# Kernel optimization log

Measured on AMD Instinct MI355X. Metric: run time of the kernel, lower is better.

Reference implementation:

```python
import jax, jax.numpy as jnp
import numpy as np

B = 2048   # batch
D = 1280   # backbone feature dim (hardcoded in module)
E = 8      # num_classes == number of expert heads
ALPHA = 0.1
EPS = 1e-5


def _bn(x, g, b, m, v):
    # BatchNorm1d in eval mode: running stats
    return (x - m) * jax.lax.rsqrt(v + EPS) * g + b


def _ln(x, g, b):
    mu = jnp.mean(x, axis=-1, keepdims=True)
    var = jnp.mean((x - mu) ** 2, axis=-1, keepdims=True)
    return (x - mu) * jax.lax.rsqrt(var + EPS) * g + b


@jax.custom_vjp
def _grad_reverse(x):
    return x

def _gr_fwd(x):
    return x, None

def _gr_bwd(_, g):
    return (-ALPHA * g,)

_grad_reverse.defvjp(_gr_fwd, _gr_bwd)


def setup_inputs() -> dict:
    key = jax.random.key(0)
    ks = iter(jax.random.split(key, 80))
    def w(*s):
        return jax.random.normal(next(ks), s, dtype=jnp.float32) * 0.02
    def u(*s):
        return jax.random.uniform(next(ks), s, dtype=jnp.float32) + 0.5
    inp = {"source": jax.random.normal(next(ks), (B, D), dtype=jnp.float32)}
    # bottleneck: Linear(1280,512)+BN+ReLU, Linear(512,256)+BN+ReLU
    inp.update(bw1=w(D, 512), bb1=jnp.zeros(512), bg1=jnp.ones(512), bbe1=jnp.zeros(512), bm1=w(512), bv1=u(512))
    inp.update(bw2=w(512, 256), bb2=jnp.zeros(256), bg2=jnp.ones(256), bbe2=jnp.zeros(256), bm2=w(256), bv2=u(256))
    # source_fc: Linear(256, E) + LogSoftmax
    inp.update(cw=w(256, E), cb=jnp.zeros(E))
    # domain classifier: 1280->1024->1024->512->2 with BN
    inp.update(dw1=w(D, 1024), db1=jnp.zeros(1024), dg1=jnp.ones(1024), dbe1=jnp.zeros(1024), dm1=w(1024), dv1=u(1024))
    inp.update(dw2=w(1024, 1024), db2=jnp.zeros(1024), dg2=jnp.ones(1024), dbe2=jnp.zeros(1024), dm2=w(1024), dv2=u(1024))
    inp.update(dw3=w(1024, 512), db3=jnp.zeros(512), dg3=jnp.ones(512), dbe3=jnp.zeros(512), dm3=w(512), dv3=u(512))
    inp.update(dw4=w(512, 2), db4=jnp.zeros(2))
    # E stacked expert MLPs: 1280->1024->1024->512->2 with LayerNorm
    inp.update(ew1=w(E, D, 1024), eb1=jnp.zeros((E, 1024)), eg1=jnp.ones((E, 1024)), ebe1=jnp.zeros((E, 1024)))
    inp.update(ew2=w(E, 1024, 1024), eb2=jnp.zeros((E, 1024)), eg2=jnp.ones((E, 1024)), ebe2=jnp.zeros((E, 1024)))
    inp.update(ew3=w(E, 1024, 512), eb3=jnp.zeros((E, 512)), eg3=jnp.ones((E, 512)), ebe3=jnp.zeros((E, 512)))
    inp.update(ew4=w(E, 512, 2), eb4=jnp.zeros((E, 2)))
    return inp


def reference(source, bw1, bb1, bg1, bbe1, bm1, bv1, bw2, bb2, bg2, bbe2, bm2, bv2, cw, cb,
              dw1, db1, dg1, dbe1, dm1, dv1, dw2, db2, dg2, dbe2, dm2, dv2,
              dw3, db3, dg3, dbe3, dm3, dv3, dw4, db4,
              ew1, eb1, eg1, ebe1, ew2, eb2, eg2, ebe2, ew3, eb3, eg3, ebe3, ew4, eb4):
    share = source  # sharedNet modeled as identity on extracted features
    # bottleneck + classifier head
    h = jax.nn.relu(_bn(share @ bw1 + bb1, bg1, bbe1, bm1, bv1))
    h = jax.nn.relu(_bn(h @ bw2 + bb2, bg2, bbe2, bm2, bv2))
    src = jax.nn.log_softmax(h @ cw + cb, axis=-1)            # [B, E]
    label = jnp.argmax(src, axis=-1)                          # routing labels (detached by argmax)
    # gradient-reversed features
    rev = _grad_reverse(share)
    # global domain classifier (dropout = identity in eval)
    d = jax.nn.relu(_bn(rev @ dw1 + db1, dg1, dbe1, dm1, dv1))
    d = jax.nn.relu(_bn(d @ dw2 + db2, dg2, dbe2, dm2, dv2))
    d = jax.nn.relu(_bn(d @ dw3 + db3, dg3, dbe3, dm3, dv3))
    dclf = jax.nn.log_softmax(d @ dw4 + db4, axis=-1)         # [B, 2]
    # per-class domain experts: dense all-expert compute + per-sample gather
    x = jax.nn.relu(_ln(jnp.einsum('bd,edh->beh', rev, ew1) + eb1[None], eg1[None], ebe1[None]))
    x = jax.nn.relu(_ln(jnp.einsum('beh,ehk->bek', x, ew2) + eb2[None], eg2[None], ebe2[None]))
    x = jax.nn.relu(_ln(jnp.einsum('beh,ehk->bek', x, ew3) + eb3[None], eg3[None], ebe3[None]))
    eo = jax.nn.log_softmax(jnp.einsum('beh,ehk->bek', x, ew4) + eb4[None], axis=-1)  # [B, E, 2]
    sout = jnp.take_along_axis(eo, label[:, None, None], axis=1)[:, 0, :]             # [B, 2]
    return (src, dclf, sout, share)
```

## Files before the change

### kernel.cpp

```cpp
#include <hip/hip_runtime.h>

typedef unsigned short u16;
typedef short s8v __attribute__((ext_vector_type(8)));
typedef float f4v __attribute__((ext_vector_type(4)));

#define AS1 __attribute__((address_space(1)))
#define AS3 __attribute__((address_space(3)))

__device__ __forceinline__ float bf2f(u16 u) {
    union { unsigned int i; float f; } x; x.i = ((unsigned int)u) << 16; return x.f;
}
__device__ __forceinline__ u16 f2bf(float f) {
    union { float f; unsigned int i; } x; x.f = f;
    unsigned int r = x.i + 0x7fffu + ((x.i >> 16) & 1u);
    return (u16)(r >> 16);
}

__device__ __forceinline__ void glds16(const u16* g, u16* l) {
    __builtin_amdgcn_global_load_lds((AS1 void*)(g), (AS3 void*)(l), 16, 0, 0);
}

__device__ __forceinline__ int swz(int row, int kq) {
    return row * 64 + ((((kq >> 3) ^ row) & 7) << 3);
}

__global__ __launch_bounds__(256) void convT2_k(const float* __restrict__ Wa,
        const float* __restrict__ Wb, int zSplit,
        u16* __restrict__ WT, int N, int K)
{
    const int z = blockIdx.z;
    const float* W = (z < zSplit) ? Wa + (size_t)z * K * N
                                  : Wb + (size_t)(z - zSplit) * K * N;
    WT += (size_t)z * K * N;
    const int n0 = blockIdx.x * 64, k0 = blockIdx.y * 64;
    __shared__ float t[64][65];
    const int r = threadIdx.x >> 2;
    const int c = (threadIdx.x & 3) << 4;
    const float* wp = W + (size_t)(k0 + r) * N + n0 + c;
    #pragma unroll
    for (int q = 0; q < 16; q += 4) {
        float4 f = *(const float4*)(wp + q);
        t[c + q + 0][r] = f.x; t[c + q + 1][r] = f.y;
        t[c + q + 2][r] = f.z; t[c + q + 3][r] = f.w;
    }
    __syncthreads();
    u16* op = WT + (size_t)(n0 + r) * K + k0 + c;
    #pragma unroll
    for (int q = 0; q < 16; q += 8) {
        s8v v;
        #pragma unroll
        for (int j = 0; j < 8; ++j) v[j] = (short)f2bf(t[r][c + q + j]);
        *(s8v*)(op + q) = v;
    }
}

__global__ __launch_bounds__(256) void convsrc_k(const float* __restrict__ in,
        u16* __restrict__ outb, float* __restrict__ outf, int n8)
{
    const int i = blockIdx.x * 256 + threadIdx.x;
    if (i >= n8) return;
    const float4 f0 = ((const float4*)in)[i * 2];
    const float4 f1 = ((const float4*)in)[i * 2 + 1];
    s8v v;
    v[0]=(short)f2bf(f0.x); v[1]=(short)f2bf(f0.y);
    v[2]=(short)f2bf(f0.z); v[3]=(short)f2bf(f0.w);
    v[4]=(short)f2bf(f1.x); v[5]=(short)f2bf(f1.y);
    v[6]=(short)f2bf(f1.z); v[7]=(short)f2bf(f1.w);
    ((s8v*)outb)[i] = v;
    ((float4*)outf)[i * 2]     = f0;
    ((float4*)outf)[i * 2 + 1] = f1;
}

template<int HASDOM>
__global__ __launch_bounds__(512) void gemm_bt128_k(
    const u16* __restrict__ A0, size_t aStrideZ,
    const u16* __restrict__ WT0,
    const float* __restrict__ ebias,
    const float* __restrict__ dbias, const float* __restrict__ dgam,
    const float* __restrict__ dbet,  const float* __restrict__ dmean,
    const float* __restrict__ dvar,  int zdom,
    u16* __restrict__ out0, int M, int N, int K)
{
    const int z = blockIdx.z;
    const u16* A  = A0  + (size_t)z * aStrideZ;
    const u16* WT = WT0 + (size_t)z * N * K;
    u16* out = out0 + (size_t)z * M * N;

    const int n0 = blockIdx.x * 128, m0 = blockIdx.y * 128;
    const int t = threadIdx.x;
    const int w = t >> 6, lane = t & 63;
    const int lq = lane >> 4, lr = lane & 15;
    const int wm = (w >> 1) * 32;
    const int wn = (w & 1) * 64;

    __shared__ __align__(16) u16 As[2 * 128 * 64];
    __shared__ __align__(16) u16 Bs[2 * 128 * 64];

    f4v acc[2][4] = {};

    const int srow = t >> 3;
    const u16* ga = A  + (size_t)(m0 + srow) * K + (((t & 7) ^ (srow & 7)) << 3);
    const u16* gb = WT + (size_t)(n0 + srow) * K + (((t & 7) ^ (srow & 7)) << 3);
    const int wq = w * 512;
    const int rowK = 64 * K;

#define STAGE(buf, kk) do { \
    glds16(ga + (kk),        As + (buf) * 8192 + wq); \
    glds16(ga + (kk) + rowK, As + (buf) * 8192 + 4096 + wq); \
    glds16(gb + (kk),        Bs + (buf) * 8192 + wq); \
    glds16(gb + (kk) + rowK, Bs + (buf) * 8192 + 4096 + wq); \
  } while (0)

    const int NT = K >> 6;
    STAGE(0, 0);
    STAGE(1, 64);

    for (int tk = 0; tk < NT; ++tk) {
        if (tk < NT - 1) asm volatile("s_waitcnt vmcnt(4)" ::: "memory");
        else             asm volatile("s_waitcnt vmcnt(0)" ::: "memory");
        __builtin_amdgcn_s_barrier();
        __builtin_amdgcn_sched_barrier(0);

        const u16* Ah = As + (tk & 1) * 8192;
        const u16* Bh = Bs + (tk & 1) * 8192;
        __builtin_amdgcn_s_setprio(1);
        #pragma unroll
        for (int ks = 0; ks < 64; ks += 32) {
            const int kq = ks + (lq << 3);
            s8v a[2], b[4];
            #pragma unroll
            for (int i = 0; i < 2; ++i) a[i] = *(const s8v*)&Ah[swz(wm + i*16 + lr, kq)];
            #pragma unroll
            for (int j = 0; j < 4; ++j) b[j] = *(const s8v*)&Bh[swz(wn + j*16 + lr, kq)];
            #pragma unroll
            for (int i = 0; i < 2; ++i)
                #pragma unroll
                for (int j = 0; j < 4; ++j)
                    acc[i][j] = __builtin_amdgcn_mfma_f32_16x16x32_bf16(a[i], b[j], acc[i][j], 0, 0, 0);
        }
        __builtin_amdgcn_s_setprio(0);
        __builtin_amdgcn_sched_barrier(0);
        __builtin_amdgcn_s_barrier();

        if (tk + 2 < NT)
            STAGE(tk & 1, (tk + 2) << 6);
    }
#undef STAGE

    float scale[4], shift[4];
    const bool dom = HASDOM && (z == zdom);
    #pragma unroll
    for (int j = 0; j < 4; ++j) {
        const int c = n0 + wn + j * 16 + lr;
        if (dom) {
            const float s = dgam[c] / sqrtf(dvar[c] + 1e-5f);
            scale[j] = s;
            shift[j] = (dbias[c] - dmean[c]) * s + dbet[c];
        } else {
            scale[j] = 1.f;
            shift[j] = ebias[(size_t)z * N + c];
        }
    }
    const int r0 = lq << 2;
    #pragma unroll
    for (int i = 0; i < 2; ++i) {
        #pragma unroll
        for (int r = 0; r < 4; ++r) {
            const int grow = m0 + wm + i * 16 + r0 + r;
            u16* orow = out + (size_t)grow * N + n0 + wn + lr;
            #pragma unroll
            for (int j = 0; j < 4; ++j) {
                float y = fmaf(acc[i][j][r], scale[j], shift[j]);
                if (dom) y = fmaxf(y, 0.f);
                orow[j * 16] = f2bf(y);
            }
        }
    }
}

__global__ __launch_bounds__(256) void gemm_f32sk_k(
    const float* __restrict__ A, const float* __restrict__ W,
    float* __restrict__ out, int M, int N, int K, int Ks)
{
    const int n0 = blockIdx.x * 128, m0 = blockIdx.y * 64;
    const int kb = blockIdx.z * Ks;
    out += (size_t)blockIdx.z * M * N;
    const int t = threadIdx.x;
    const int tx = t & 15, ty = t >> 4;
    __shared__ float As[64 * 33];
    __shared__ float Bs[32 * 132];
    float acc[4][8] = {};
    const int ar = t >> 2, akc = (t & 3) * 8;
    const int bk = t >> 3, bnc = (t & 7) * 16;
    for (int kk = kb; kk < kb + Ks; kk += 32) {
        const float* ap = A + (size_t)(m0 + ar) * K + kk + akc;
        const float4 fa0 = *(const float4*)(ap);
        const float4 fa1 = *(const float4*)(ap + 4);
        float* asp = &As[ar * 33 + akc];
        asp[0] = fa0.x; asp[1] = fa0.y; asp[2] = fa0.z; asp[3] = fa0.w;
        asp[4] = fa1.x; asp[5] = fa1.y; asp[6] = fa1.z; asp[7] = fa1.w;
        const float* wp = W + (size_t)(kk + bk) * N + n0 + bnc;
        #pragma unroll
        for (int q = 0; q < 4; ++q)
            *(float4*)&Bs[bk * 132 + bnc + q * 4] = *(const float4*)(wp + q * 4);
        __syncthreads();
        #pragma unroll 8
        for (int kq = 0; kq < 32; ++kq) {
            float a[4];
            #pragma unroll
            for (int i = 0; i < 4; ++i) a[i] = As[(ty + 16 * i) * 33 + kq];
            const float4 b0 = *(const float4*)&Bs[kq * 132 + tx * 4];
            const float4 b1 = *(const float4*)&Bs[kq * 132 + tx * 4 + 64];
            #pragma unroll
            for (int i = 0; i < 4; ++i) {
                acc[i][0] = fmaf(a[i], b0.x, acc[i][0]);
                acc[i][1] = fmaf(a[i], b0.y, acc[i][1]);
                acc[i][2] = fmaf(a[i], b0.z, acc[i][2]);
                acc[i][3] = fmaf(a[i], b0.w, acc[i][3]);
                acc[i][4] = fmaf(a[i], b1.x, acc[i][4]);
                acc[i][5] = fmaf(a[i], b1.y, acc[i][5]);
                acc[i][6] = fmaf(a[i], b1.z, acc[i][6]);
                acc[i][7] = fmaf(a[i], b1.w, acc[i][7]);
            }
        }
        __syncthreads();
    }
    #pragma unroll
    for (int i = 0; i < 4; ++i) {
        float* orow = out + (size_t)(m0 + ty + 16 * i) * N + n0 + tx * 4;
        float4 o0; o0.x = acc[i][0]; o0.y = acc[i][1]; o0.z = acc[i][2]; o0.w = acc[i][3];
        float4 o1; o1.x = acc[i][4]; o1.y = acc[i][5]; o1.z = acc[i][6]; o1.w = acc[i][7];
        *(float4*)orow = o0;
        *(float4*)(orow + 64) = o1;
    }
}

__global__ __launch_bounds__(256) void h2gemm_k(
    const float* __restrict__ hp,
    const float* __restrict__ bg1, const float* __restrict__ bbe1,
    const float* __restrict__ bb1, const float* __restrict__ bm1,
    const float* __restrict__ bv1,
    const float* __restrict__ bw2,
    float* __restrict__ out, int B)
{
    const int n0 = blockIdx.x * 64, m0 = blockIdx.y * 64;
    const int kb = blockIdx.z * 128;
    out += (size_t)blockIdx.z * B * 256;
    const size_t sl = (size_t)B * 512;
    const int tid = threadIdx.x;
    const int tx = tid & 15, ty = tid >> 4;
    __shared__ float As[64][65];
    __shared__ float Bs[64][64];
    __shared__ __align__(16) float scl[128], shl[128];
    if (tid < 128) {
        const int k = kb + tid;
        const float sc = bg1[k] / sqrtf(bv1[k] + 1e-5f);
        scl[tid] = sc;
        shl[tid] = (bb1[k] - bm1[k]) * sc + bbe1[k];
    }
    __syncthreads();
    float acc[4][4] = {};
    const int sr = tid >> 2;
    const int sc = (tid & 3) << 4;
    for (int kk = kb; kk < kb + 128; kk += 64) {
        const int kl = kk - kb;
        const float* ap = hp + (size_t)(m0 + sr) * 512 + kk + sc;
        #pragma unroll
        for (int q = 0; q < 4; ++q) {
            float vx = 0.f, vy = 0.f, vz = 0.f, vw = 0.f;
            #pragma unroll
            for (int s = 0; s < 8; ++s) {
                const float4 f = *(const float4*)(ap + (size_t)s * sl + q * 4);
                vx += f.x; vy += f.y; vz += f.z; vw += f.w;
            }
            const float4 g = *(const float4*)&scl[kl + sc + q * 4];
            const float4 h = *(const float4*)&shl[kl + sc + q * 4];
            As[sr][sc + q*4 + 0] = fmaxf(fmaf(vx, g.x, h.x), 0.f);
            As[sr][sc + q*4 + 1] = fmaxf(fmaf(vy, g.y, h.y), 0.f);
            As[sr][sc + q*4 + 2] = fmaxf(fmaf(vz, g.z, h.z), 0.f);
            As[sr][sc + q*4 + 3] = fmaxf(fmaf(vw, g.w, h.w), 0.f);
        }
        const float* wp = bw2 + (size_t)(kk + sr) * 256 + n0 + sc;
        #pragma unroll
        for (int q = 0; q < 4; ++q)
            *(float4*)&Bs[sr][sc + q*4] = *(const float4*)(wp + q * 4);
        __syncthreads();
        #pragma unroll 4
        for (int kq = 0; kq < 64; ++kq) {
            float a[4], bv[4];
            #pragma unroll
            for (int i = 0; i < 4; ++i) a[i] = As[ty*4 + i][kq];
            #pragma unroll
            for (int j = 0; j < 4; ++j) bv[j] = Bs[kq][tx*4 + j];
            #pragma unroll
            for (int i = 0; i < 4; ++i)
                #pragma unroll
                for (int j = 0; j < 4; ++j)
                    acc[i][j] = fmaf(a[i], bv[j], acc[i][j]);
        }
        __syncthreads();
    }
    #pragma unroll
    for (int j = 0; j < 4; ++j) {
        const int c = n0 + tx*4 + j;
        #pragma unroll
        for (int i = 0; i < 4; ++i)
            out[(size_t)(m0 + ty*4 + i) * 256 + c] = acc[i][j];
    }
}

__global__ __launch_bounds__(256) void cls_k(
    const float* __restrict__ h2p,
    const float* __restrict__ bg2, const float* __restrict__ bbe2,
    const float* __restrict__ bb2, const float* __restrict__ bm2,
    const float* __restrict__ bv2,
    const float* __restrict__ cw,  const float* __restrict__ cb,
    float* __restrict__ out_src, int* __restrict__ label, int B)
{
    const int b = blockIdx.x * 4 + (threadIdx.x >> 6);
    const int lane = threadIdx.x & 63;
    const size_t sl = (size_t)B * 256;
    const float* hb = h2p + (size_t)b * 256 + lane * 4;
    const float4 v0 = *(const float4*)(hb);
    const float4 v1 = *(const float4*)(hb + sl);
    const float4 v2 = *(const float4*)(hb + 2 * sl);
    const float4 v3 = *(const float4*)(hb + 3 * sl);
    const float4 gv = ((const float4*)bg2)[lane];
    const float4 vv = ((const float4*)bv2)[lane];
    const float4 bbv = ((const float4*)bb2)[lane];
    const float4 bmv = ((const float4*)bm2)[lane];
    const float4 bev = ((const float4*)bbe2)[lane];
    float h[4];
    {
        const float s0 = gv.x / sqrtf(vv.x + 1e-5f);
        const float s1 = gv.y / sqrtf(vv.y + 1e-5f);
        const float s2 = gv.z / sqrtf(vv.z + 1e-5f);
        const float s3 = gv.w / sqrtf(vv.w + 1e-5f);
        h[0] = fmaxf(fmaf(v0.x + v1.x + v2.x + v3.x, s0, (bbv.x - bmv.x) * s0 + bev.x), 0.f);
        h[1] = fmaxf(fmaf(v0.y + v1.y + v2.y + v3.y, s1, (bbv.y - bmv.y) * s1 + bev.y), 0.f);
        h[2] = fmaxf(fmaf(v0.z + v1.z + v2.z + v3.z, s2, (bbv.z - bmv.z) * s2 + bev.z), 0.f);
        h[3] = fmaxf(fmaf(v0.w + v1.w + v2.w + v3.w, s3, (bbv.w - bmv.w) * s3 + bev.w), 0.f);
    }
    float p[8] = {};
    #pragma unroll
    for (int j = 0; j < 4; ++j) {
        const float4 c0 = ((const float4*)cw)[(lane * 4 + j) * 2];
        const float4 c1 = ((const float4*)cw)[(lane * 4 + j) * 2 + 1];
        p[0] = fmaf(h[j], c0.x, p[0]); p[1] = fmaf(h[j], c0.y, p[1]);
        p[2] = fmaf(h[j], c0.z, p[2]); p[3] = fmaf(h[j], c0.w, p[3]);
        p[4] = fmaf(h[j], c1.x, p[4]); p[5] = fmaf(h[j], c1.y, p[5]);
        p[6] = fmaf(h[j], c1.z, p[6]); p[7] = fmaf(h[j], c1.w, p[7]);
    }
    #pragma unroll
    for (int off = 32; off; off >>= 1)
        #pragma unroll
        for (int c = 0; c < 8; ++c) p[c] += __shfl_xor(p[c], off, 64);
    if (lane == 0) {
        float lg[8];
        #pragma unroll
        for (int c = 0; c < 8; ++c) lg[c] = p[c] + cb[c];
        float mx = lg[0]; int am = 0;
        #pragma unroll
        for (int c = 1; c < 8; ++c) if (lg[c] > mx) { mx = lg[c]; am = c; }
        float ssum = 0.f;
        #pragma unroll
        for (int c = 0; c < 8; ++c) ssum += expf(lg[c] - mx);
        const float lse = mx + logf(ssum);
        #pragma unroll
        for (int c = 0; c < 8; ++c) out_src[b * 8 + c] = lg[c] - lse;
        label[b] = am;
    }
}

template<int N>
__global__ __launch_bounds__(256) void ln_relu_k(u16* __restrict__ Y,
        const float* __restrict__ g, const float* __restrict__ bb)
{
    const int z = blockIdx.y;
    u16* y = Y + ((size_t)z * gridDim.x + blockIdx.x) * N;
    const float* gz = g  + (size_t)z * N;
    const float* bz = bb + (size_t)z * N;
    const int t = threadIdx.x;
    constexpr int C = N >> 8;
    float vals[C];
    ushort4 u = ((const ushort4*)y)[t];
    vals[0] = bf2f(u.x); vals[1] = bf2f(u.y);
    vals[2] = bf2f(u.z); vals[3] = bf2f(u.w);
    float s = 0.f, sq = 0.f;
    #pragma unroll
    for (int i = 0; i < C; ++i) { s += vals[i]; sq += vals[i] * vals[i]; }
    #pragma unroll
    for (int off = 32; off; off >>= 1) {
        s  += __shfl_xor(s,  off, 64);
        sq += __shfl_xor(sq, off, 64);
    }
    __shared__ float rs[4], rq[4];
    if ((t & 63) == 0) { rs[t >> 6] = s; rq[t >> 6] = sq; }
    __syncthreads();
    s  = rs[0] + rs[1] + rs[2] + rs[3];
    sq = rq[0] + rq[1] + rq[2] + rq[3];
    const float inv = 1.f / (float)N;
    const float mu  = s * inv;
    const float var = sq * inv - mu * mu;
    const float rstd = rsqrtf(var + 1e-5f);
    float4 gv = ((const float4*)gz)[t];
    float4 bv = ((const float4*)bz)[t];
    ushort4 o;
    o.x = f2bf(fmaxf((vals[0] - mu) * rstd * gv.x + bv.x, 0.f));
    o.y = f2bf(fmaxf((vals[1] - mu) * rstd * gv.y + bv.y, 0.f));
    o.z = f2bf(fmaxf((vals[2] - mu) * rstd * gv.z + bv.z, 0.f));
    o.w = f2bf(fmaxf((vals[3] - mu) * rstd * gv.w + bv.w, 0.f));
    ((ushort4*)y)[t] = o;
}

__global__ __launch_bounds__(64) void headsel_k(
    const u16* __restrict__ X,
    const int* __restrict__ label,
    const float* __restrict__ eg3, const float* __restrict__ ebe3,
    const float* __restrict__ ew4, const float* __restrict__ eb4,
    int zBase, float* __restrict__ out_sout, int B)
{
    const int b = blockIdx.x;
    const int e = label[b];
    if (e < zBase || e >= zBase + 4) return;
    const int lane = threadIdx.x;
    const u16* x = X + ((size_t)(e - zBase) * B + b) * 512 + lane * 8;
    uint4 raw = *(const uint4*)x;
    const u16* pu = (const u16*)&raw;
    float v[8];
    #pragma unroll
    for (int i = 0; i < 8; ++i) v[i] = bf2f(pu[i]);
    float s = 0.f, sq = 0.f;
    #pragma unroll
    for (int i = 0; i < 8; ++i) { s += v[i]; sq += v[i] * v[i]; }
    #pragma unroll
    for (int off = 32; off; off >>= 1) {
        s  += __shfl_xor(s,  off, 64);
        sq += __shfl_xor(sq, off, 64);
    }
    const float mu = s * (1.f / 512.f);
    const float var = sq * (1.f / 512.f) - mu * mu;
    const float rstd = rsqrtf(var + 1e-5f);
    const float* g  = eg3  + (size_t)e * 512 + lane * 8;
    const float* be = ebe3 + (size_t)e * 512 + lane * 8;
    const float4 g0 = *(const float4*)g,  g1 = *(const float4*)(g + 4);
    const float4 b0 = *(const float4*)be, b1 = *(const float4*)(be + 4);
    float h[8];
    h[0] = fmaxf((v[0]-mu)*rstd*g0.x + b0.x, 0.f);
    h[1] = fmaxf((v[1]-mu)*rstd*g0.y + b0.y, 0.f);
    h[2] = fmaxf((v[2]-mu)*rstd*g0.z + b0.z, 0.f);
    h[3] = fmaxf((v[3]-mu)*rstd*g0.w + b0.w, 0.f);
    h[4] = fmaxf((v[4]-mu)*rstd*g1.x + b1.x, 0.f);
    h[5] = fmaxf((v[5]-mu)*rstd*g1.y + b1.y, 0.f);
    h[6] = fmaxf((v[6]-mu)*rstd*g1.z + b1.z, 0.f);
    h[7] = fmaxf((v[7]-mu)*rstd*g1.w + b1.w, 0.f);
    const float* W = ew4 + (size_t)e * 1024 + lane * 16;
    float p0 = 0.f, p1 = 0.f;
    #pragma unroll
    for (int q = 0; q < 4; ++q) {
        const float4 wv = *(const float4*)(W + q * 4);
        p0 = fmaf(h[q*2],   wv.x, p0); p1 = fmaf(h[q*2],   wv.y, p1);
        p0 = fmaf(h[q*2+1], wv.z, p0); p1 = fmaf(h[q*2+1], wv.w, p1);
    }
    #pragma unroll
    for (int off = 32; off; off >>= 1) {
        p0 += __shfl_xor(p0, off, 64);
        p1 += __shfl_xor(p1, off, 64);
    }
    if (lane == 0) {
        const float l0 = p0 + eb4[e * 2];
        const float l1 = p1 + eb4[e * 2 + 1];
        const float mx = fmaxf(l0, l1);
        const float lse = mx + logf(expf(l0 - mx) + expf(l1 - mx));
        out_sout[b * 2]     = l0 - lse;
        out_sout[b * 2 + 1] = l1 - lse;
    }
}

__global__ __launch_bounds__(64) void head2_k(const u16* __restrict__ X,
        const float* __restrict__ W, const float* __restrict__ bias,
        float* __restrict__ out)
{
    const int b = blockIdx.x;
    const int lane = threadIdx.x;
    const u16* x = X + (size_t)b * 512 + lane * 8;
    uint4 raw = *(const uint4*)x;
    const u16* pu = (const u16*)&raw;
    const float* Wz = W + lane * 16;
    float p0 = 0.f, p1 = 0.f;
    #pragma unroll
    for (int q = 0; q < 4; ++q) {
        const float4 wv = *(const float4*)(Wz + q * 4);
        p0 = fmaf(bf2f(pu[q*2]),   wv.x, p0); p1 = fmaf(bf2f(pu[q*2]),   wv.y, p1);
        p0 = fmaf(bf2f(pu[q*2+1]), wv.z, p0); p1 = fmaf(bf2f(pu[q*2+1]), wv.w, p1);
    }
    #pragma unroll
    for (int off = 32; off; off >>= 1) {
        p0 += __shfl_xor(p0, off, 64);
        p1 += __shfl_xor(p1, off, 64);
    }
    if (lane == 0) {
        const float l0 = p0 + bias[0];
        const float l1 = p1 + bias[1];
        const float mx = fmaxf(l0, l1);
        const float lse = mx + logf(expf(l0 - mx) + expf(l1 - mx));
        out[b * 2]     = l0 - lse;
        out[b * 2 + 1] = l1 - lse;
    }
}


extern "C" void kernel_launch(void* const* d_in, const int* in_sizes, int n_in,
                              void* d_out, int out_size, void* d_ws, size_t ws_size,
                              hipStream_t stream)
{
    const int B = 2048, D = 1280, E = 8;

    const float* src = (const float*)d_in[0];
    const float *bw1 = (const float*)d_in[1],  *bb1 = (const float*)d_in[2],
                *bg1 = (const float*)d_in[3],  *bbe1 = (const float*)d_in[4],
                *bm1 = (const float*)d_in[5],  *bv1 = (const float*)d_in[6];
    const float *bw2 = (const float*)d_in[7],  *bb2 = (const float*)d_in[8],
                *bg2 = (const float*)d_in[9],  *bbe2 = (const float*)d_in[10],
                *bm2 = (const float*)d_in[11], *bv2 = (const float*)d_in[12];
    const float *cw  = (const float*)d_in[13], *cb  = (const float*)d_in[14];
    const float *dw1 = (const float*)d_in[15], *db1 = (const float*)d_in[16],
                *dg1 = (const float*)d_in[17], *dbe1 = (const float*)d_in[18],
                *dm1 = (const float*)d_in[19], *dv1 = (const float*)d_in[20];
    const float *dw2 = (const float*)d_in[21], *db2 = (const float*)d_in[22],
                *dg2 = (const float*)d_in[23], *dbe2 = (const float*)d_in[24],
                *dm2 = (const float*)d_in[25], *dv2 = (const float*)d_in[26];
    const float *dw3 = (const float*)d_in[27], *db3 = (const float*)d_in[28],
                *dg3 = (const float*)d_in[29], *dbe3 = (const float*)d_in[30],
                *dm3 = (const float*)d_in[31], *dv3 = (const float*)d_in[32];
    const float *dw4 = (const float*)d_in[33], *db4 = (const float*)d_in[34];
    const float *ew1 = (const float*)d_in[35], *eb1 = (const float*)d_in[36],
                *eg1 = (const float*)d_in[37], *ebe1 = (const float*)d_in[38];
    const float *ew2 = (const float*)d_in[39], *eb2 = (const float*)d_in[40],
                *eg2 = (const float*)d_in[41], *ebe2 = (const float*)d_in[42];
    const float *ew3 = (const float*)d_in[43], *eb3 = (const float*)d_in[44],
                *eg3 = (const float*)d_in[45], *ebe3 = (const float*)d_in[46];
    const float *ew4 = (const float*)d_in[47], *eb4 = (const float*)d_in[48];

    float* out_src   = (float*)d_out;
    float* out_dclf  = out_src + B * E;
    float* out_sout  = out_dclf + B * 2;
    float* out_share = out_sout + B * 2;

    char* ws = (char*)d_ws;
    u16*   wslot = (u16*)ws;
    u16*   srcb  = (u16*)(ws + 13107200);
    u16*   acta  = (u16*)(ws + 18350080);
    u16*   actb  = (u16*)(ws + 39321600);
    int*   label = (int*)(ws + 60293120);
    float* hp    = (float*)(ws + 18350080);
    float* h2p   = (float*)(ws);

    const size_t s1024 = (size_t)B * 1024, s512 = (size_t)B * 512;

    convsrc_k<<<dim3(B * D / 8 / 256), 256, 0, stream>>>(src, srcb, out_share, B * D / 8);

    gemm_f32sk_k<<<dim3(512 / 128, B / 64, 8), 256, 0, stream>>>(
        src, bw1, hp, B, 512, D, 160);
    h2gemm_k<<<dim3(256 / 64, B / 64, 4), 256, 0, stream>>>(
        hp, bg1, bbe1, bb1, bm1, bv1, bw2, h2p, B);
    cls_k<<<dim3(B / 4), 256, 0, stream>>>(
        h2p, bg2, bbe2, bb2, bm2, bv2, cw, cb, out_src, label, B);

    convT2_k<<<dim3(16, 20, 5), 256, 0, stream>>>(ew1, dw1, 4, wslot, 1024, 1280);
    gemm_bt128_k<1><<<dim3(8, 16, 5), 512, 0, stream>>>(
        srcb, 0, wslot, eb1, db1, dg1, dbe1, dm1, dv1, 4, acta, B, 1024, 1280);
    ln_relu_k<1024><<<dim3(B, 4), 256, 0, stream>>>(acta, eg1, ebe1);

    convT2_k<<<dim3(16, 16, 5), 256, 0, stream>>>(ew2, dw2, 4, wslot, 1024, 1024);
    gemm_bt128_k<1><<<dim3(8, 16, 5), 512, 0, stream>>>(
        acta, s1024, wslot, eb2, db2, dg2, dbe2, dm2, dv2, 4, actb, B, 1024, 1024);
    ln_relu_k<1024><<<dim3(B, 4), 256, 0, stream>>>(actb, eg2, ebe2);

    convT2_k<<<dim3(8, 16, 5), 256, 0, stream>>>(ew3, dw3, 4, wslot, 512, 1024);
    gemm_bt128_k<1><<<dim3(4, 16, 5), 512, 0, stream>>>(
        actb, s1024, wslot, eb3, db3, dg3, dbe3, dm3, dv3, 4, acta, B, 512, 1024);

    headsel_k<<<dim3(B), 64, 0, stream>>>(
        acta, label, eg3, ebe3, ew4, eb4, 0, out_sout, B);
    head2_k<<<dim3(B), 64, 0, stream>>>(
        acta + (size_t)4 * s512, dw4, db4, out_dclf);

    convT2_k<<<dim3(16, 20, 4), 256, 0, stream>>>(
        ew1 + (size_t)4*1280*1024, ew1 + (size_t)4*1280*1024, 4, wslot, 1024, 1280);
    gemm_bt128_k<0><<<dim3(8, 16, 4), 512, 0, stream>>>(
        srcb, 0, wslot, eb1 + (size_t)4*1024,
        nullptr, nullptr, nullptr, nullptr, nullptr, -1, acta, B, 1024, 1280);
    ln_relu_k<1024><<<dim3(B, 4), 256, 0, stream>>>(acta, eg1 + (size_t)4*1024, ebe1 + (size_t)4*1024);

    convT2_k<<<dim3(16, 16, 4), 256, 0, stream>>>(
        ew2 + (size_t)4*1024*1024, ew2 + (size_t)4*1024*1024, 4, wslot, 1024, 1024);
    gemm_bt128_k<0><<<dim3(8, 16, 4), 512, 0, stream>>>(
        acta, s1024, wslot, eb2 + (size_t)4*1024,
        nullptr, nullptr, nullptr, nullptr, nullptr, -1, actb, B, 1024, 1024);
    ln_relu_k<1024><<<dim3(B, 4), 256, 0, stream>>>(actb, eg2 + (size_t)4*1024, ebe2 + (size_t)4*1024);

    convT2_k<<<dim3(8, 16, 4), 256, 0, stream>>>(
        ew3 + (size_t)4*1024*512, ew3 + (size_t)4*1024*512, 4, wslot, 512, 1024);
    gemm_bt128_k<0><<<dim3(4, 16, 4), 512, 0, stream>>>(
        actb, s1024, wslot, eb3 + (size_t)4*512,
        nullptr, nullptr, nullptr, nullptr, nullptr, -1, acta, B, 512, 1024);

    headsel_k<<<dim3(B), 64, 0, stream>>>(
        acta, label, eg3, ebe3, ew4, eb4, 4, out_sout, B);
}
```

Before: 555.3 us.

## Fuse fp32 weight transpose/bf16 conversion into GEMM B-tile loading

Removes the separate convT2_k pre-pass that transposed and converted fp32 weights to bf16 in workspace. The GEMM now reads fp32 weights directly from global memory into registers, converts them to bf16 and writes them into swizzled LDS, with the A tile still loaded asynchronously via global_load_lds. This saves six extra launches and the write and re-read of the bf16 weight copies. In exchange, the pipeline is shallower (one tile ahead instead of two), the strided scalar fp32 loads are each re-read by all 16 M-blocks, and conversion work sits on the GEMM's critical path.

```diff
diff --git a/kernel.cpp b/kernel.cpp
--- a/kernel.cpp
+++ b/kernel.cpp
@@ -22,36 +22,6 @@
 
 __device__ __forceinline__ int swz(int row, int kq) {
     return row * 64 + ((((kq >> 3) ^ row) & 7) << 3);
-}
-
-__global__ __launch_bounds__(256) void convT2_k(const float* __restrict__ Wa,
-        const float* __restrict__ Wb, int zSplit,
-        u16* __restrict__ WT, int N, int K)
-{
-    const int z = blockIdx.z;
-    const float* W = (z < zSplit) ? Wa + (size_t)z * K * N
-                                  : Wb + (size_t)(z - zSplit) * K * N;
-    WT += (size_t)z * K * N;
-    const int n0 = blockIdx.x * 64, k0 = blockIdx.y * 64;
-    __shared__ float t[64][65];
-    const int r = threadIdx.x >> 2;
-    const int c = (threadIdx.x & 3) << 4;
-    const float* wp = W + (size_t)(k0 + r) * N + n0 + c;
-    #pragma unroll
-    for (int q = 0; q < 16; q += 4) {
-        float4 f = *(const float4*)(wp + q);
-        t[c + q + 0][r] = f.x; t[c + q + 1][r] = f.y;
-        t[c + q + 2][r] = f.z; t[c + q + 3][r] = f.w;
-    }
-    __syncthreads();
-    u16* op = WT + (size_t)(n0 + r) * K + k0 + c;
-    #pragma unroll
-    for (int q = 0; q < 16; q += 8) {
-        s8v v;
-        #pragma unroll
-        for (int j = 0; j < 8; ++j) v[j] = (short)f2bf(t[r][c + q + j]);
-        *(s8v*)(op + q) = v;
-    }
 }
 
 __global__ __launch_bounds__(256) void convsrc_k(const float* __restrict__ in,
@@ -72,9 +42,9 @@
 }
 
 template<int HASDOM>
-__global__ __launch_bounds__(512) void gemm_bt128_k(
+__global__ __launch_bounds__(512) void gemm_btf_k(
     const u16* __restrict__ A0, size_t aStrideZ,
-    const u16* __restrict__ WT0,
+    const float* __restrict__ Wa, const float* __restrict__ Wb, int zSplit,
     const float* __restrict__ ebias,
     const float* __restrict__ dbias, const float* __restrict__ dgam,
     const float* __restrict__ dbet,  const float* __restrict__ dmean,
@@ -82,8 +52,9 @@
     u16* __restrict__ out0, int M, int N, int K)
 {
     const int z = blockIdx.z;
-    const u16* A  = A0  + (size_t)z * aStrideZ;
-    const u16* WT = WT0 + (size_t)z * N * K;
+    const u16* A = A0 + (size_t)z * aStrideZ;
+    const float* W = (z < zSplit) ? Wa + (size_t)z * K * N
+                                  : Wb + (size_t)(z - zSplit) * K * N;
     u16* out = out0 + (size_t)z * M * N;
 
     const int n0 = blockIdx.x * 128, m0 = blockIdx.y * 128;
@@ -93,36 +64,62 @@
     const int wm = (w >> 1) * 32;
     const int wn = (w & 1) * 64;
 
-    __shared__ __align__(16) u16 As[2 * 128 * 64];
-    __shared__ __align__(16) u16 Bs[2 * 128 * 64];
+    __shared__ __align__(16) u16 As[2 * 8192];
+    __shared__ __align__(16) u16 Bs[2 * 8192];
 
     f4v acc[2][4] = {};
 
     const int srow = t >> 3;
-    const u16* ga = A  + (size_t)(m0 + srow) * K + (((t & 7) ^ (srow & 7)) << 3);
-    const u16* gb = WT + (size_t)(n0 + srow) * K + (((t & 7) ^ (srow & 7)) << 3);
+    const u16* ga = A + (size_t)(m0 + srow) * K + (((t & 7) ^ (srow & 7)) << 3);
     const int wq = w * 512;
     const int rowK = 64 * K;
 
-#define STAGE(buf, kk) do { \
+#define AGLDS(buf, kk) do { \
     glds16(ga + (kk),        As + (buf) * 8192 + wq); \
-    glds16(ga + (kk) + rowK, As + (buf) * 8192 + 4096 + wq); \
-    glds16(gb + (kk),        Bs + (buf) * 8192 + wq); \
-    glds16(gb + (kk) + rowK, Bs + (buf) * 8192 + 4096 + wq); \
-  } while (0)
+    glds16(ga + (kk) + rowK, As + (buf) * 8192 + 4096 + wq); } while (0)
+
+    const int nl = t & 127;
+    const int kb = (t >> 7) << 4;
+    const float* wp0 = W + (size_t)kb * N + n0 + nl;
+    const int bofs0 = nl * 64 + (((( kb >> 3)      ^ nl) & 7) << 3);
+    const int bofs1 = nl * 64 + (((((kb >> 3) + 1) ^ nl) & 7) << 3);
 
     const int NT = K >> 6;
-    STAGE(0, 0);
-    STAGE(1, 64);
+    float bv[16];
+
+    {
+        #pragma unroll
+        for (int i = 0; i < 16; ++i) bv[i] = wp0[(size_t)i * N];
+        AGLDS(0, 0);
+        s8v pk0, pk1;
+        #pragma unroll
+        for (int i = 0; i < 8; ++i) { pk0[i] = (short)f2bf(bv[i]); pk1[i] = (short)f2bf(bv[8 + i]); }
+        *(s8v*)&Bs[bofs0] = pk0;
+        *(s8v*)&Bs[bofs1] = pk1;
+    }
 
     for (int tk = 0; tk < NT; ++tk) {
-        if (tk < NT - 1) asm volatile("s_waitcnt vmcnt(4)" ::: "memory");
-        else             asm volatile("s_waitcnt vmcnt(0)" ::: "memory");
+        const int cur = tk & 1;
+        if (tk + 1 < NT) {
+            const float* wp = wp0 + (size_t)(tk + 1) * 64 * N;
+            #pragma unroll
+            for (int i = 0; i < 16; ++i) bv[i] = wp[(size_t)i * N];
+            AGLDS(cur ^ 1, (tk + 1) << 6);
+            s8v pk0, pk1;
+            #pragma unroll
+            for (int i = 0; i < 8; ++i) { pk0[i] = (short)f2bf(bv[i]); pk1[i] = (short)f2bf(bv[8 + i]); }
+            u16* bb = Bs + (cur ^ 1) * 8192;
+            *(s8v*)&bb[bofs0] = pk0;
+            *(s8v*)&bb[bofs1] = pk1;
+        } else {
+            asm volatile("s_waitcnt vmcnt(0)" ::: "memory");
+        }
+        asm volatile("s_waitcnt lgkmcnt(0)" ::: "memory");
         __builtin_amdgcn_s_barrier();
         __builtin_amdgcn_sched_barrier(0);
 
-        const u16* Ah = As + (tk & 1) * 8192;
-        const u16* Bh = Bs + (tk & 1) * 8192;
+        const u16* Ah = As + cur * 8192;
+        const u16* Bh = Bs + cur * 8192;
         __builtin_amdgcn_s_setprio(1);
         #pragma unroll
         for (int ks = 0; ks < 64; ks += 32) {
@@ -141,11 +138,8 @@
         __builtin_amdgcn_s_setprio(0);
         __builtin_amdgcn_sched_barrier(0);
         __builtin_amdgcn_s_barrier();
-
-        if (tk + 2 < NT)
-            STAGE(tk & 1, (tk + 2) << 6);
-    }
-#undef STAGE
+    }
+#undef AGLDS
 
     float scale[4], shift[4];
     const bool dom = HASDOM && (z == zdom);
@@ -548,7 +542,6 @@
     float* out_share = out_sout + B * 2;
 
     char* ws = (char*)d_ws;
-    u16*   wslot = (u16*)ws;
     u16*   srcb  = (u16*)(ws + 13107200);
     u16*   acta  = (u16*)(ws + 18350080);
     u16*   actb  = (u16*)(ws + 39321600);
@@ -567,44 +560,38 @@
     cls_k<<<dim3(B / 4), 256, 0, stream>>>(
         h2p, bg2, bbe2, bb2, bm2, bv2, cw, cb, out_src, label, B);
 
-    convT2_k<<<dim3(16, 20, 5), 256, 0, stream>>>(ew1, dw1, 4, wslot, 1024, 1280);
-    gemm_bt128_k<1><<<dim3(8, 16, 5), 512, 0, stream>>>(
-        srcb, 0, wslot, eb1, db1, dg1, dbe1, dm1, dv1, 4, acta, B, 1024, 1280);
+    gemm_btf_k<1><<<dim3(8, 16, 5), 512, 0, stream>>>(
+        srcb, 0, ew1, dw1, 4, eb1, db1, dg1, dbe1, dm1, dv1, 4, acta, B, 1024, 1280);
     ln_relu_k<1024><<<dim3(B, 4), 256, 0, stream>>>(acta, eg1, ebe1);
 
-    convT2_k<<<dim3(16, 16, 5), 256, 0, stream>>>(ew2, dw2, 4, wslot, 1024, 1024);
-    gemm_bt128_k<1><<<dim3(8, 16, 5), 512, 0, stream>>>(
-        acta, s1024, wslot, eb2, db2, dg2, dbe2, dm2, dv2, 4, actb, B, 1024, 1024);
+    gemm_btf_k<1><<<dim3(8, 16, 5), 512, 0, stream>>>(
+        acta, s1024, ew2, dw2, 4, eb2, db2, dg2, dbe2, dm2, dv2, 4, actb, B, 1024, 1024);
     ln_relu_k<1024><<<dim3(B, 4), 256, 0, stream>>>(actb, eg2, ebe2);
 
-    convT2_k<<<dim3(8, 16, 5), 256, 0, stream>>>(ew3, dw3, 4, wslot, 512, 1024);
-    gemm_bt128_k<1><<<dim3(4, 16, 5), 512, 0, stream>>>(
-        actb, s1024, wslot, eb3, db3, dg3, dbe3, dm3, dv3, 4, acta, B, 512, 1024);
+    gemm_btf_k<1><<<dim3(4, 16, 5), 512, 0, stream>>>(
+        actb, s1024, ew3, dw3, 4, eb3, db3, dg3, dbe3, dm3, dv3, 4, acta, B, 512, 1024);
 
     headsel_k<<<dim3(B), 64, 0, stream>>>(
         acta, label, eg3, ebe3, ew4, eb4, 0, out_sout, B);
     head2_k<<<dim3(B), 64, 0, stream>>>(
         acta + (size_t)4 * s512, dw4, db4, out_dclf);
 
-    convT2_k<<<dim3(16, 20, 4), 256, 0, stream>>>(
-        ew1 + (size_t)4*1280*1024, ew1 + (size_t)4*1280*1024, 4, wslot, 1024, 1280);
-    gemm_bt128_k<0><<<dim3(8, 16, 4), 512, 0, stream>>>(
-        srcb, 0, wslot, eb1 + (size_t)4*1024,
-        nullptr, nullptr, nullptr, nullptr, nullptr, -1, acta, B, 1024, 1280);
+    gemm_btf_k<0><<<dim3(8, 16, 4), 512, 0, stream>>>(
+        srcb, 0, ew1 + (size_t)4*1280*1024, ew1 + (size_t)4*1280*1024, 4,
+        eb1 + (size_t)4*1024, nullptr, nullptr, nullptr, nullptr, nullptr, -1,
+        acta, B, 1024, 1280);
     ln_relu_k<1024><<<dim3(B, 4), 256, 0, stream>>>(acta, eg1 + (size_t)4*1024, ebe1 + (size_t)4*1024);
 
-    convT2_k<<<dim3(16, 16, 4), 256, 0, stream>>>(
-        ew2 + (size_t)4*1024*1024, ew2 + (size_t)4*1024*1024, 4, wslot, 1024, 1024);
-    gemm_bt128_k<0><<<dim3(8, 16, 4), 512, 0, stream>>>(
-        acta, s1024, wslot, eb2 + (size_t)4*1024,
-        nullptr, nullptr, nullptr, nullptr, nullptr, -1, actb, B, 1024, 1024);
+    gemm_btf_k<0><<<dim3(8, 16, 4), 512, 0, stream>>>(
+        acta, s1024, ew2 + (size_t)4*1024*1024, ew2 + (size_t)4*1024*1024, 4,
+        eb2 + (size_t)4*1024, nullptr, nullptr, nullptr, nullptr, nullptr, -1,
+        actb, B, 1024, 1024);
     ln_relu_k<1024><<<dim3(B, 4), 256, 0, stream>>>(actb, eg2 + (size_t)4*1024, ebe2 + (size_t)4*1024);
 
-    convT2_k<<<dim3(8, 16, 4), 256, 0, stream>>>(
-        ew3 + (size_t)4*1024*512, ew3 + (size_t)4*1024*512, 4, wslot, 512, 1024);
-    gemm_bt128_k<0><<<dim3(4, 16, 4), 512, 0, stream>>>(
-        actb, s1024, wslot, eb3 + (size_t)4*512,
-        nullptr, nullptr, nullptr, nullptr, nullptr, -1, acta, B, 512, 1024);
+    gemm_btf_k<0><<<dim3(4, 16, 4), 512, 0, stream>>>(
+        actb, s1024, ew3 + (size_t)4*1024*512, ew3 + (size_t)4*1024*512, 4,
+        eb3 + (size_t)4*512, nullptr, nullptr, nullptr, nullptr, nullptr, -1,
+        acta, B, 512, 1024);
 
     headsel_k<<<dim3(B), 64, 0, stream>>>(
         acta, label, eg3, ebe3, ew4, eb4, 4, out_sout, B);
```

New measurement: 632.4 us. 13.9% more time.
